# Kernel tuning notes

Hardware: AMD Instinct MI355X
Metric: run time of the kernel (lower is better)

## Reference

```python
import jax, jax.numpy as jnp
import numpy as np

N, E, IN, HID, HEADS, OUT = 50000, 800000, 128, 32, 4, 2
NEG = 0.2   # LeakyReLU negative slope (PyG default)
EPS = 1e-5  # BatchNorm eps


def setup_inputs() -> dict:
    key = jax.random.key(0)
    ks = jax.random.split(key, 32)
    g = lambda i, shape, s=0.05: (jax.random.normal(ks[i], shape, jnp.float32) * s)
    d = {
        'x': jax.random.normal(ks[0], (N, IN), jnp.float32),
        'edge_index': jax.random.randint(ks[1], (2, E), 0, N, jnp.int32),
        'edge_attr': jax.random.normal(ks[2], (E, 1), jnp.float32),
        # conv1: GATv2, in=IN, out=HID, heads=HEADS, edge_dim=1
        'c1_Wl': g(3, (IN, HEADS * HID)), 'c1_bl': g(4, (HEADS * HID,)),
        'c1_Wr': g(5, (IN, HEADS * HID)), 'c1_br': g(6, (HEADS * HID,)),
        'c1_We': g(7, (1, HEADS * HID)),
        'c1_att': g(8, (HEADS, HID)),
        'c1_bias': g(9, (HEADS * HID,)),
        'bn1_gamma': jnp.ones((HEADS * HID,), jnp.float32),
        'bn1_beta': jnp.zeros((HEADS * HID,), jnp.float32),
        'bn1_mean': g(10, (HEADS * HID,)),
        'bn1_var': jax.random.uniform(ks[11], (HEADS * HID,), jnp.float32, 0.5, 1.5),
        # conv2: GATv2, in=HEADS*HID, out=HID, heads=1, edge_dim=1
        'c2_Wl': g(12, (HEADS * HID, HID)), 'c2_bl': g(13, (HID,)),
        'c2_Wr': g(14, (HEADS * HID, HID)), 'c2_br': g(15, (HID,)),
        'c2_We': g(16, (1, HID)),
        'c2_att': g(17, (1, HID)),
        'c2_bias': g(18, (HID,)),
        'bn2_gamma': jnp.ones((HID,), jnp.float32),
        'bn2_beta': jnp.zeros((HID,), jnp.float32),
        'bn2_mean': g(19, (HID,)),
        'bn2_var': jax.random.uniform(ks[20], (HID,), jnp.float32, 0.5, 1.5),
        # classifier
        'clf_W': g(21, (HID, OUT)), 'clf_b': g(22, (OUT,)),
    }
    return d


def _gatv2(x, src, dst, eattr, Wl, bl, Wr, br, We, att, bias, heads, out_ch, concat):
    n = x.shape[0]
    xl = (x @ Wl + bl).reshape(n, heads, out_ch)   # source transform
    xr = (x @ Wr + br).reshape(n, heads, out_ch)   # target transform
    el = (eattr @ We).reshape(-1, heads, out_ch)   # edge transform (no bias in PyG)
    s = xl[src] + xr[dst] + el                     # [E, H, C]
    s = jnp.where(s > 0, s, NEG * s)               # LeakyReLU
    logits = jnp.einsum('ehc,hc->eh', s, att)      # [E, H]
    # segment softmax over destination nodes (every node has a self-loop)
    m = jax.ops.segment_max(logits, dst, num_segments=n)
    a = jnp.exp(logits - m[dst])
    denom = jax.ops.segment_sum(a, dst, num_segments=n)
    alpha = a / denom[dst]                         # [E, H]
    out = jax.ops.segment_sum(alpha[:, :, None] * xl[src], dst, num_segments=n)
    out = out.reshape(n, heads * out_ch) if concat else out.mean(axis=1)
    return out + bias


def _bn_eval(x, gamma, beta, mean, var):
    return (x - mean) * (gamma / jnp.sqrt(var + EPS)) + beta


def reference(x, edge_index, edge_attr,
              c1_Wl, c1_bl, c1_Wr, c1_br, c1_We, c1_att, c1_bias,
              bn1_gamma, bn1_beta, bn1_mean, bn1_var,
              c2_Wl, c2_bl, c2_Wr, c2_br, c2_We, c2_att, c2_bias,
              bn2_gamma, bn2_beta, bn2_mean, bn2_var,
              clf_W, clf_b):
    n = x.shape[0]
    # add self-loops once (PyG GATv2 default add_self_loops=True, fill_value='mean')
    loop = jnp.arange(n, dtype=edge_index.dtype)
    src = jnp.concatenate([edge_index[0], loop])
    dst = jnp.concatenate([edge_index[1], loop])
    loop_attr = jnp.broadcast_to(edge_attr.mean(axis=0, keepdims=True), (n, edge_attr.shape[1]))
    eattr = jnp.concatenate([edge_attr, loop_attr], axis=0)

    h = _gatv2(x, src, dst, eattr, c1_Wl, c1_bl, c1_Wr, c1_br, c1_We, c1_att, c1_bias,
               HEADS, HID, True)
    h = jax.nn.relu(_bn_eval(h, bn1_gamma, bn1_beta, bn1_mean, bn1_var))
    # dropout inactive in eval mode
    h = _gatv2(h, src, dst, eattr, c2_Wl, c2_bl, c2_Wr, c2_br, c2_We, c2_att, c2_bias,
               1, HID, True)
    h = jax.nn.relu(_bn_eval(h, bn2_gamma, bn2_beta, bn2_mean, bn2_var))
    return h @ clf_W + clf_b
```

## Files before the change

kernel.cpp:

```cpp
#include <hip/hip_runtime.h>

#define NNODES 50000
#define NEDGES 800000
#define ETOT   850000
#define IN_CH  128
#define HID    32
#define C1     128
#define NEG    0.2f
#define BNEPS  1e-5f
#define XFB2   1563
#define EHB    3125
#define WTS    160
#define XSS    136
#define NC     16
#define SCB    196

typedef __attribute__((ext_vector_type(8))) short short8;
typedef __attribute__((ext_vector_type(4))) float f32x4;

__device__ __forceinline__ unsigned short bf16r(float f) {
    unsigned u = __float_as_uint(f);
    return (unsigned short)((u + 0x7fffu + ((u >> 16) & 1u)) >> 16);
}
__device__ __forceinline__ unsigned bf16pair(float f0, float f1) {
    return (unsigned)bf16r(f0) | ((unsigned)bf16r(f1) << 16);
}
__device__ __forceinline__ float blo(unsigned u) { return __uint_as_float(u << 16); }
__device__ __forceinline__ float bhi(unsigned u) { return __uint_as_float(u & 0xffff0000u); }

__device__ __forceinline__ int block_iscan(int v, int* ls) {
    int lane = threadIdx.x & 63, w = threadIdx.x >> 6;
    #pragma unroll
    for (int o = 1; o < 64; o <<= 1) {
        int t = __shfl_up(v, o);
        if (lane >= o) v += t;
    }
    if (lane == 63) ls[w] = v;
    __syncthreads();
    int add = 0;
    #pragma unroll
    for (int i = 0; i < 4; i++) add += (i < w) ? ls[i] : 0;
    return v + add;
}

__global__ __launch_bounds__(256) void k_prep(const float* __restrict__ Wl1,
                                              const float* __restrict__ Wr1,
                                              const float* __restrict__ Wl2,
                                              const float* __restrict__ Wr2,
                                              unsigned short* __restrict__ WT,
                                              unsigned short* __restrict__ WT2,
                                              int* __restrict__ hist,
                                              float* __restrict__ meanbuf) {
    int idx = blockIdx.x * 256 + threadIdx.x;
    if (idx == 0) meanbuf[0] = 0.f;
    for (int i = idx; i < NC * NNODES; i += 160 * 256) hist[i] = 0;
    if (idx < 32768) {
        int mat = idx >> 14, rem = idx & 16383;
        int k = rem >> 7, n = rem & 127;
        float v = mat ? Wr1[k * 128 + n] : Wl1[k * 128 + n];
        WT[(size_t)(mat * 128 + n) * WTS + k] = bf16r(v);
    } else {
        int i2 = idx - 32768;
        int mat = i2 >> 12, rem = i2 & 4095;
        int k = rem >> 5, n = rem & 31;
        float v = mat ? Wr2[k * 32 + n] : Wl2[k * 32 + n];
        WT2[(size_t)(mat * 32 + n) * WTS + k] = bf16r(v);
    }
}

__global__ __launch_bounds__(256) void k_xf_eh(
    const float* __restrict__ x,
    const float* __restrict__ bl, const float* __restrict__ br,
    const unsigned short* __restrict__ WT,
    unsigned* __restrict__ xlb, float* __restrict__ xr,
    const int* __restrict__ ei, const float* __restrict__ ea,
    int* __restrict__ hist, int* __restrict__ eoff,
    float* __restrict__ meanbuf) {
    __shared__ short xs_s[64 * XSS];
    int bi = blockIdx.x;
    if (bi % 3 != 0) {
        float* ls = (float*)xs_s;
        int hb = bi - bi / 3 - 1;
        if (hb >= EHB) return;
        int e = hb * 256 + threadIdx.x;
        int c = hb & (NC - 1);
        float v = 0.f;
        if (e < NEDGES) {
            eoff[e] = atomicAdd(&hist[c * NNODES + ei[NEDGES + e]], 1);
            v = ea[e];
        }
        #pragma unroll
        for (int o = 32; o > 0; o >>= 1) v += __shfl_down(v, o, 64);
        if ((threadIdx.x & 63) == 0) ls[threadIdx.x >> 6] = v;
        __syncthreads();
        if (threadIdx.x == 0) atomicAdd(meanbuf, ls[0] + ls[1] + ls[2] + ls[3]);
        return;
    }
    int n0g = (bi / 3) * 32;
    {
        int nd = threadIdx.x >> 3, kc = (threadIdx.x & 7) * 16;
        bool valid = (n0g + nd) < NNODES;
        float xv[16];
        #pragma unroll
        for (int i = 0; i < 4; i++) {
            float4 t = valid ? ((const float4*)(x + (size_t)(n0g + nd) * IN_CH + kc))[i]
                             : make_float4(0.f, 0.f, 0.f, 0.f);
            xv[4 * i] = t.x; xv[4 * i + 1] = t.y; xv[4 * i + 2] = t.z; xv[4 * i + 3] = t.w;
        }
        unsigned hi[8], lo[8];
        #pragma unroll
        for (int i = 0; i < 8; i++) {
            unsigned short h0 = bf16r(xv[2 * i]), h1 = bf16r(xv[2 * i + 1]);
            float l0 = xv[2 * i]     - __uint_as_float(((unsigned)h0) << 16);
            float l1 = xv[2 * i + 1] - __uint_as_float(((unsigned)h1) << 16);
            hi[i] = (unsigned)h0 | ((unsigned)h1 << 16);
            lo[i] = bf16pair(l0, l1);
        }
        uint4* ph = (uint4*)&xs_s[nd * XSS + kc];
        ph[0] = make_uint4(hi[0], hi[1], hi[2], hi[3]);
        ph[1] = make_uint4(hi[4], hi[5], hi[6], hi[7]);
        uint4* pl = (uint4*)&xs_s[(nd + 32) * XSS + kc];
        pl[0] = make_uint4(lo[0], lo[1], lo[2], lo[3]);
        pl[1] = make_uint4(lo[4], lo[5], lo[6], lo[7]);
    }
    __syncthreads();
    int lane = threadIdx.x & 63;
    int lm = lane & 15, q = lane >> 4;
    int w = threadIdx.x >> 6;
    int n0 = w * 64;
    f32x4 acc[2][4];
    #pragma unroll
    for (int mt = 0; mt < 2; mt++)
        #pragma unroll
        for (int nt = 0; nt < 4; nt++) acc[mt][nt] = (f32x4)0.f;

    #pragma unroll
    for (int ks = 0; ks < 4; ks++) {
        int k0 = ks * 32 + q * 8;
        short8 ah0 = *(const short8*)&xs_s[(lm)      * XSS + k0];
        short8 ah1 = *(const short8*)&xs_s[(16 + lm) * XSS + k0];
        short8 al0 = *(const short8*)&xs_s[(32 + lm) * XSS + k0];
        short8 al1 = *(const short8*)&xs_s[(48 + lm) * XSS + k0];
        #pragma unroll
        for (int nt = 0; nt < 4; nt++) {
            short8 bfr = *(const short8*)(WT + (size_t)(n0 + nt * 16 + lm) * WTS + k0);
            acc[0][nt] = __builtin_amdgcn_mfma_f32_16x16x32_bf16(al0, bfr, acc[0][nt], 0, 0, 0);
            acc[0][nt] = __builtin_amdgcn_mfma_f32_16x16x32_bf16(ah0, bfr, acc[0][nt], 0, 0, 0);
            acc[1][nt] = __builtin_amdgcn_mfma_f32_16x16x32_bf16(al1, bfr, acc[1][nt], 0, 0, 0);
            acc[1][nt] = __builtin_amdgcn_mfma_f32_16x16x32_bf16(ah1, bfr, acc[1][nt], 0, 0, 0);
        }
    }
    if (w < 2) {
        #pragma unroll
        for (int nt = 0; nt < 4; nt++) {
            int ch = n0 + nt * 16 + lm;
            float bv = bl[ch];
            #pragma unroll
            for (int mt = 0; mt < 2; mt++)
                #pragma unroll
                for (int r = 0; r < 4; r++) {
                    int node = n0g + mt * 16 + q * 4 + r;
                    float val = acc[mt][nt][r] + bv;
                    float pv = __shfl_xor(val, 1);
                    if ((lm & 1) == 0 && node < NNODES)
                        xlb[(size_t)node * 64 + (ch >> 1)] = bf16pair(val, pv);
                }
        }
    } else {
        #pragma unroll
        for (int nt = 0; nt < 4; nt++) {
            int ch = n0 - 128 + nt * 16 + lm;
            float bv = br[ch];
            #pragma unroll
            for (int mt = 0; mt < 2; mt++)
                #pragma unroll
                for (int r = 0; r < 4; r++) {
                    int node = n0g + mt * 16 + q * 4 + r;
                    if (node < NNODES)
                        xr[(size_t)node * C1 + ch] = acc[mt][nt][r] + bv;
                }
        }
    }
}

__global__ __launch_bounds__(256) void k_red(int* __restrict__ hist,
                                             int* __restrict__ deg,
                                             int* __restrict__ bsum) {
    __shared__ int ls[4];
    int d = blockIdx.x * 256 + threadIdx.x;
    int s = 0;
    if (d < NNODES) {
        #pragma unroll
        for (int c = 0; c < NC; c++) {
            int v = hist[c * NNODES + d];
            hist[c * NNODES + d] = s;
            s += v;
        }
        deg[d] = s;
    }
    int v = (d < NNODES) ? s + 1 : 0;
    #pragma unroll
    for (int o = 32; o > 0; o >>= 1) v += __shfl_down(v, o, 64);
    if ((threadIdx.x & 63) == 0) ls[threadIdx.x >> 6] = v;
    __syncthreads();
    if (threadIdx.x == 0) bsum[blockIdx.x] = ls[0] + ls[1] + ls[2] + ls[3];
}

__global__ __launch_bounds__(256) void k_rowp(const int* __restrict__ deg,
                                              const int* __restrict__ bsum,
                                              int* __restrict__ rowptr) {
    __shared__ int ls[4];
    int t = threadIdx.x;
    int bv = (t < SCB) ? bsum[t] : 0;
    int bincl = block_iscan(bv, ls);
    __shared__ int boffs[256];
    boffs[t] = bincl - bv;
    __syncthreads();
    int base = boffs[blockIdx.x];
    __syncthreads();
    int d = blockIdx.x * 256 + t;
    int v = (d < NNODES) ? deg[d] + 1 : 0;
    int incl = block_iscan(v, ls);
    if (d < NNODES) rowptr[d] = base + incl - v;
    if (d == NNODES - 1) rowptr[NNODES] = base + incl;
}

__global__ __launch_bounds__(256) void k_fill(const int* __restrict__ ei,
                                              const float* __restrict__ ea,
                                              const int* __restrict__ rowptr,
                                              const float* __restrict__ meanbuf,
                                              const int* __restrict__ hist,
                                              const int* __restrict__ eoff,
                                              unsigned* __restrict__ cpack) {
    int e = blockIdx.x * 256 + threadIdx.x;
    if (e < NEDGES) {
        int d = ei[NEDGES + e];
        int c = (e >> 8) & (NC - 1);
        int pos = rowptr[d] + 1 + hist[c * NNODES + d] + eoff[e];
        cpack[pos] = ((unsigned)bf16r(ea[e]) << 16) | (unsigned)ei[e];
    } else if (e < NEDGES + NNODES) {
        int i = e - NEDGES;
        cpack[rowptr[i]] = ((unsigned)bf16r(meanbuf[0] * (1.0f / NEDGES)) << 16) | (unsigned)i;
    } else if (e < NEDGES + NNODES + 64) {
        cpack[ETOT + e - NEDGES - NNODES] = 0u;
    }
}

__global__ __launch_bounds__(256) void k_edge1(
    const unsigned* __restrict__ xlb, const float* __restrict__ xr,
    const int* __restrict__ rowptr, const unsigned* __restrict__ cpack,
    const float* __restrict__ We, const float* __restrict__ att,
    float* __restrict__ out1) {
    int node = blockIdx.x * 4 + (threadIdx.x >> 6);
    if (node >= NNODES) return;
    int lane = threadIdx.x & 63;
    int q = lane & 15, s = lane >> 4;
    int r0 = rowptr[node], r1 = rowptr[node + 1];
    float4 xr0 = ((const float4*)xr)[(size_t)node * 32 + 2 * q];
    float4 xr1 = ((const float4*)xr)[(size_t)node * 32 + 2 * q + 1];
    float4 we0 = ((const float4*)We)[2 * q],  we1 = ((const float4*)We)[2 * q + 1];
    float4 at0 = ((const float4*)att)[2 * q], at1 = ((const float4*)att)[2 * q + 1];
    const uint4* xlv = (const uint4*)xlb;

    float den = 0.f;
    float a0 = 0.f, a1 = 0.f, a2 = 0.f, a3 = 0.f;
    float a4 = 0.f, a5 = 0.f, a6 = 0.f, a7 = 0.f;
    int nit = (r1 - r0 + 3) >> 2;
    int k = r0 + s;
    unsigned sc0 = cpack[k];
    uint4 xv0 = xlv[(size_t)(sc0 & 0xffffu) * 16 + q];
    unsigned sc1 = cpack[k + 4];
    uint4 xv1 = xlv[(size_t)(sc1 & 0xffffu) * 16 + q];
    for (int it = 0; it < nit; it++) {
        unsigned scn = cpack[k + 8];
        uint4 xvn = xlv[(size_t)(scn & 0xffffu) * 16 + q];
        bool ok = k < r1;
        float av = __uint_as_float(sc0 & 0xffff0000u);
        float x0 = blo(xv0.x), x1 = bhi(xv0.x), x2 = blo(xv0.y), x3 = bhi(xv0.y);
        float x4 = blo(xv0.z), x5 = bhi(xv0.z), x6 = blo(xv0.w), x7 = bhi(xv0.w);
        float v0 = x0 + xr0.x + av * we0.x;  v0 = v0 > 0.f ? v0 : NEG * v0;
        float v1 = x1 + xr0.y + av * we0.y;  v1 = v1 > 0.f ? v1 : NEG * v1;
        float v2 = x2 + xr0.z + av * we0.z;  v2 = v2 > 0.f ? v2 : NEG * v2;
        float v3 = x3 + xr0.w + av * we0.w;  v3 = v3 > 0.f ? v3 : NEG * v3;
        float v4 = x4 + xr1.x + av * we1.x;  v4 = v4 > 0.f ? v4 : NEG * v4;
        float v5 = x5 + xr1.y + av * we1.y;  v5 = v5 > 0.f ? v5 : NEG * v5;
        float v6 = x6 + xr1.z + av * we1.z;  v6 = v6 > 0.f ? v6 : NEG * v6;
        float v7 = x7 + xr1.w + av * we1.w;  v7 = v7 > 0.f ? v7 : NEG * v7;
        float t = v0 * at0.x + v1 * at0.y + v2 * at0.z + v3 * at0.w
                + v4 * at1.x + v5 * at1.y + v6 * at1.z + v7 * at1.w;
        t += __shfl_xor(t, 1);
        t += __shfl_xor(t, 2);
        float e = ok ? __expf(t) : 0.f;
        den += e;
        a0 = fmaf(e, x0, a0); a1 = fmaf(e, x1, a1);
        a2 = fmaf(e, x2, a2); a3 = fmaf(e, x3, a3);
        a4 = fmaf(e, x4, a4); a5 = fmaf(e, x5, a5);
        a6 = fmaf(e, x6, a6); a7 = fmaf(e, x7, a7);
        k += 4;
        sc0 = sc1; xv0 = xv1;
        sc1 = scn; xv1 = xvn;
    }
    #pragma unroll
    for (int o = 16; o <= 32; o <<= 1) {
        den += __shfl_xor(den, o);
        a0 += __shfl_xor(a0, o); a1 += __shfl_xor(a1, o);
        a2 += __shfl_xor(a2, o); a3 += __shfl_xor(a3, o);
        a4 += __shfl_xor(a4, o); a5 += __shfl_xor(a5, o);
        a6 += __shfl_xor(a6, o); a7 += __shfl_xor(a7, o);
    }
    if (s == 0) {
        float rd = 1.f / den;
        ((float4*)out1)[(size_t)node * 32 + 2 * q] =
            make_float4(a0 * rd, a1 * rd, a2 * rd, a3 * rd);
        ((float4*)out1)[(size_t)node * 32 + 2 * q + 1] =
            make_float4(a4 * rd, a5 * rd, a6 * rd, a7 * rd);
    }
}

__global__ __launch_bounds__(256) void k_epi(
    const float* __restrict__ out1, const float* __restrict__ bias1,
    const float* __restrict__ g1, const float* __restrict__ b1,
    const float* __restrict__ m1, const float* __restrict__ v1,
    const unsigned short* __restrict__ WT2,
    const float* __restrict__ bl2, const float* __restrict__ br2,
    unsigned* __restrict__ xlb2, float* __restrict__ xr2) {
    __shared__ short hs_s[64 * XSS];
    __shared__ float A[128], B[128];
    int n0g = blockIdx.x * 32;
    if (threadIdx.x < 128) {
        int c = threadIdx.x;
        float sc = g1[c] * rsqrtf(v1[c] + BNEPS);
        A[c] = sc;
        B[c] = (bias1[c] - m1[c]) * sc + b1[c];
    }
    __syncthreads();
    {
        int nd = threadIdx.x >> 3, kc = (threadIdx.x & 7) * 16;
        bool valid = (n0g + nd) < NNODES;
        float xv[16];
        #pragma unroll
        for (int i = 0; i < 4; i++) {
            float4 t = valid ? ((const float4*)(out1 + (size_t)(n0g + nd) * C1 + kc))[i]
                             : make_float4(0.f, 0.f, 0.f, 0.f);
            xv[4 * i] = t.x; xv[4 * i + 1] = t.y; xv[4 * i + 2] = t.z; xv[4 * i + 3] = t.w;
        }
        #pragma unroll
        for (int j = 0; j < 16; j++)
            xv[j] = fmaxf(xv[j] * A[kc + j] + B[kc + j], 0.f);
        unsigned hi[8], lo[8];
        #pragma unroll
        for (int i = 0; i < 8; i++) {
            unsigned short h0 = bf16r(xv[2 * i]), h1 = bf16r(xv[2 * i + 1]);
            float l0 = xv[2 * i]     - __uint_as_float(((unsigned)h0) << 16);
            float l1 = xv[2 * i + 1] - __uint_as_float(((unsigned)h1) << 16);
            hi[i] = (unsigned)h0 | ((unsigned)h1 << 16);
            lo[i] = bf16pair(l0, l1);
        }
        uint4* ph = (uint4*)&hs_s[nd * XSS + kc];
        ph[0] = make_uint4(hi[0], hi[1], hi[2], hi[3]);
        ph[1] = make_uint4(hi[4], hi[5], hi[6], hi[7]);
        uint4* pl = (uint4*)&hs_s[(nd + 32) * XSS + kc];
        pl[0] = make_uint4(lo[0], lo[1], lo[2], lo[3]);
        pl[1] = make_uint4(lo[4], lo[5], lo[6], lo[7]);
    }
    __syncthreads();
    int lane = threadIdx.x & 63;
    int lm = lane & 15, q = lane >> 4;
    int w = threadIdx.x >> 6;
    f32x4 acc[2];
    acc[0] = (f32x4)0.f; acc[1] = (f32x4)0.f;
    #pragma unroll
    for (int ks = 0; ks < 4; ks++) {
        int k0 = ks * 32 + q * 8;
        short8 ah0 = *(const short8*)&hs_s[(lm)      * XSS + k0];
        short8 ah1 = *(const short8*)&hs_s[(16 + lm) * XSS + k0];
        short8 al0 = *(const short8*)&hs_s[(32 + lm) * XSS + k0];
        short8 al1 = *(const short8*)&hs_s[(48 + lm) * XSS + k0];
        short8 bfr = *(const short8*)(WT2 + (size_t)(w * 16 + lm) * WTS + k0);
        acc[0] = __builtin_amdgcn_mfma_f32_16x16x32_bf16(al0, bfr, acc[0], 0, 0, 0);
        acc[0] = __builtin_amdgcn_mfma_f32_16x16x32_bf16(ah0, bfr, acc[0], 0, 0, 0);
        acc[1] = __builtin_amdgcn_mfma_f32_16x16x32_bf16(al1, bfr, acc[1], 0, 0, 0);
        acc[1] = __builtin_amdgcn_mfma_f32_16x16x32_bf16(ah1, bfr, acc[1], 0, 0, 0);
    }
    if (w < 2) {
        int ch = w * 16 + lm;
        float bv = bl2[ch];
        #pragma unroll
        for (int mt = 0; mt < 2; mt++)
            #pragma unroll
            for (int r = 0; r < 4; r++) {
                int node = n0g + mt * 16 + q * 4 + r;
                float val = acc[mt][r] + bv;
                float pv = __shfl_xor(val, 1);
                if ((lm & 1) == 0 && node < NNODES)
                    xlb2[(size_t)node * 16 + (ch >> 1)] = bf16pair(val, pv);
            }
    } else {
        int ch = (w - 2) * 16 + lm;
        float bv = br2[ch];
        #pragma unroll
        for (int mt = 0; mt < 2; mt++)
            #pragma unroll
            for (int r = 0; r < 4; r++) {
                int node = n0g + mt * 16 + q * 4 + r;
                if (node < NNODES)
                    xr2[(size_t)node * HID + ch] = acc[mt][r] + bv;
            }
    }
}

__global__ __launch_bounds__(256) void k_edge2(
    const unsigned* __restrict__ xlb2, const float* __restrict__ xr2,
    const int* __restrict__ rowptr, const unsigned* __restrict__ cpack,
    const float* __restrict__ We2, const float* __restrict__ att2,
    const float* __restrict__ bias2,
    const float* __restrict__ g2, const float* __restrict__ b2,
    const float* __restrict__ m2, const float* __restrict__ v2,
    const float* __restrict__ W, const float* __restrict__ b,
    float* __restrict__ y) {
    int node = blockIdx.x * 4 + (threadIdx.x >> 6);
    if (node >= NNODES) return;
    int lane = threadIdx.x & 63;
    int q = lane & 3, s = lane >> 2;
    int r0 = rowptr[node], r1 = rowptr[node + 1];
    float4 xr0 = ((const float4*)xr2)[(size_t)node * 8 + 2 * q];
    float4 xr1 = ((const float4*)xr2)[(size_t)node * 8 + 2 * q + 1];
    float4 we0 = ((const float4*)We2)[2 * q],  we1 = ((const float4*)We2)[2 * q + 1];
    float4 at0 = ((const float4*)att2)[2 * q], at1 = ((const float4*)att2)[2 * q + 1];
    const uint4* xlv = (const uint4*)xlb2;

    float den = 0.f;
    float a0 = 0.f, a1 = 0.f, a2 = 0.f, a3 = 0.f;
    float a4 = 0.f, a5 = 0.f, a6 = 0.f, a7 = 0.f;
    int nit = (r1 - r0 + 15) >> 4;
    int k = r0 + s;
    unsigned sc = cpack[k];
    uint4 xv = xlv[(size_t)(sc & 0xffffu) * 4 + q];
    for (int it = 0; it < nit; it++) {
        unsigned scn = cpack[k + 16];
        uint4 xvn = xlv[(size_t)(scn & 0xffffu) * 4 + q];
        bool ok = k < r1;
        float av = __uint_as_float(sc & 0xffff0000u);
        float x0 = blo(xv.x), x1 = bhi(xv.x), x2 = blo(xv.y), x3 = bhi(xv.y);
        float x4 = blo(xv.z), x5 = bhi(xv.z), x6 = blo(xv.w), x7 = bhi(xv.w);
        float v0 = x0 + xr0.x + av * we0.x;  v0 = v0 > 0.f ? v0 : NEG * v0;
        float v1 = x1 + xr0.y + av * we0.y;  v1 = v1 > 0.f ? v1 : NEG * v1;
        float v2 = x2 + xr0.z + av * we0.z;  v2 = v2 > 0.f ? v2 : NEG * v2;
        float v3 = x3 + xr0.w + av * we0.w;  v3 = v3 > 0.f ? v3 : NEG * v3;
        float v4 = x4 + xr1.x + av * we1.x;  v4 = v4 > 0.f ? v4 : NEG * v4;
        float v5 = x5 + xr1.y + av * we1.y;  v5 = v5 > 0.f ? v5 : NEG * v5;
        float v6 = x6 + xr1.z + av * we1.z;  v6 = v6 > 0.f ? v6 : NEG * v6;
        float v7 = x7 + xr1.w + av * we1.w;  v7 = v7 > 0.f ? v7 : NEG * v7;
        float t = v0 * at0.x + v1 * at0.y + v2 * at0.z + v3 * at0.w
                + v4 * at1.x + v5 * at1.y + v6 * at1.z + v7 * at1.w;
        t += __shfl_xor(t, 1);
        t += __shfl_xor(t, 2);
        float e = ok ? __expf(t) : 0.f;
        den += e;
        a0 = fmaf(e, x0, a0); a1 = fmaf(e, x1, a1);
        a2 = fmaf(e, x2, a2); a3 = fmaf(e, x3, a3);
        a4 = fmaf(e, x4, a4); a5 = fmaf(e, x5, a5);
        a6 = fmaf(e, x6, a6); a7 = fmaf(e, x7, a7);
        k += 16; sc = scn; xv = xvn;
    }
    #pragma unroll
    for (int o = 4; o <= 32; o <<= 1) {
        den += __shfl_xor(den, o);
        a0 += __shfl_xor(a0, o); a1 += __shfl_xor(a1, o);
        a2 += __shfl_xor(a2, o); a3 += __shfl_xor(a3, o);
        a4 += __shfl_xor(a4, o); a5 += __shfl_xor(a5, o);
        a6 += __shfl_xor(a6, o); a7 += __shfl_xor(a7, o);
    }
    float rd = 1.f / den;
    float4 gv0 = ((const float4*)g2)[2 * q],    gv1 = ((const float4*)g2)[2 * q + 1];
    float4 bv0 = ((const float4*)b2)[2 * q],    bv1 = ((const float4*)b2)[2 * q + 1];
    float4 mv0 = ((const float4*)m2)[2 * q],    mv1 = ((const float4*)m2)[2 * q + 1];
    float4 vv0 = ((const float4*)v2)[2 * q],    vv1 = ((const float4*)v2)[2 * q + 1];
    float4 bi0 = ((const float4*)bias2)[2 * q], bi1 = ((const float4*)bias2)[2 * q + 1];
    float h0 = (a0 * rd + bi0.x - mv0.x) * (gv0.x * rsqrtf(vv0.x + BNEPS)) + bv0.x;
    float h1 = (a1 * rd + bi0.y - mv0.y) * (gv0.y * rsqrtf(vv0.y + BNEPS)) + bv0.y;
    float h2 = (a2 * rd + bi0.z - mv0.z) * (gv0.z * rsqrtf(vv0.z + BNEPS)) + bv0.z;
    float h3 = (a3 * rd + bi0.w - mv0.w) * (gv0.w * rsqrtf(vv0.w + BNEPS)) + bv0.w;
    float h4 = (a4 * rd + bi1.x - mv1.x) * (gv1.x * rsqrtf(vv1.x + BNEPS)) + bv1.x;
    float h5 = (a5 * rd + bi1.y - mv1.y) * (gv1.y * rsqrtf(vv1.y + BNEPS)) + bv1.y;
    float h6 = (a6 * rd + bi1.z - mv1.z) * (gv1.z * rsqrtf(vv1.z + BNEPS)) + bv1.z;
    float h7 = (a7 * rd + bi1.w - mv1.w) * (gv1.w * rsqrtf(vv1.w + BNEPS)) + bv1.w;
    h0 = fmaxf(h0, 0.f); h1 = fmaxf(h1, 0.f); h2 = fmaxf(h2, 0.f); h3 = fmaxf(h3, 0.f);
    h4 = fmaxf(h4, 0.f); h5 = fmaxf(h5, 0.f); h6 = fmaxf(h6, 0.f); h7 = fmaxf(h7, 0.f);
    float4 w0 = ((const float4*)W)[4 * q];
    float4 w1 = ((const float4*)W)[4 * q + 1];
    float4 w2 = ((const float4*)W)[4 * q + 2];
    float4 w3 = ((const float4*)W)[4 * q + 3];
    float t0 = h0 * w0.x + h1 * w0.z + h2 * w1.x + h3 * w1.z
             + h4 * w2.x + h5 * w2.z + h6 * w3.x + h7 * w3.z;
    float t1 = h0 * w0.y + h1 * w0.w + h2 * w1.y + h3 * w1.w
             + h4 * w2.y + h5 * w2.w + h6 * w3.y + h7 * w3.w;
    t0 += __shfl_xor(t0, 1); t0 += __shfl_xor(t0, 2);
    t1 += __shfl_xor(t1, 1); t1 += __shfl_xor(t1, 2);
    if (lane == 0) {
        y[(size_t)node * 2]     = t0 + b[0];
        y[(size_t)node * 2 + 1] = t1 + b[1];
    }
}

extern "C" void kernel_launch(void* const* d_in, const int* in_sizes, int n_in,
                              void* d_out, int out_size, void* d_ws, size_t ws_size,
                              hipStream_t stream) {
    const float* x       = (const float*)d_in[0];
    const int*   ei      = (const int*)d_in[1];
    const float* ea      = (const float*)d_in[2];
    const float* c1_Wl   = (const float*)d_in[3];
    const float* c1_bl   = (const float*)d_in[4];
    const float* c1_Wr   = (const float*)d_in[5];
    const float* c1_br   = (const float*)d_in[6];
    const float* c1_We   = (const float*)d_in[7];
    const float* c1_att  = (const float*)d_in[8];
    const float* c1_bias = (const float*)d_in[9];
    const float* bn1_g   = (const float*)d_in[10];
    const float* bn1_b   = (const float*)d_in[11];
    const float* bn1_m   = (const float*)d_in[12];
    const float* bn1_v   = (const float*)d_in[13];
    const float* c2_Wl   = (const float*)d_in[14];
    const float* c2_bl   = (const float*)d_in[15];
    const float* c2_Wr   = (const float*)d_in[16];
    const float* c2_br   = (const float*)d_in[17];
    const float* c2_We   = (const float*)d_in[18];
    const float* c2_att  = (const float*)d_in[19];
    const float* c2_bias = (const float*)d_in[20];
    const float* bn2_g   = (const float*)d_in[21];
    const float* bn2_b   = (const float*)d_in[22];
    const float* bn2_m   = (const float*)d_in[23];
    const float* bn2_v   = (const float*)d_in[24];
    const float* clf_W   = (const float*)d_in[25];
    const float* clf_b   = (const float*)d_in[26];

    float* ws = (float*)d_ws;
    size_t off = 0;
    unsigned* XLb  = (unsigned*)(ws + off); off += (size_t)NNODES * 64;
    float*    XR1  = ws + off; off += (size_t)NNODES * C1;
    float*    OUT1 = ws + off; off += (size_t)NNODES * C1;
    unsigned* XLb2 = (unsigned*)(ws + off); off += (size_t)NNODES * 16;
    float*    XR2  = ws + off; off += (size_t)NNODES * HID;
    unsigned* CPACK= (unsigned*)(ws + off); off += (size_t)ETOT + 64;
    unsigned short* WT  = (unsigned short*)(ws + off); off += 256 * WTS / 2;
    unsigned short* WT2 = (unsigned short*)(ws + off); off += 64 * WTS / 2;
    int*      EOFF = (int*)(ws + off); off += NEDGES;
    int*      ROWP = (int*)(ws + off); off += NNODES + 16;
    int*      DEG  = (int*)(ws + off); off += NNODES;
    int*      BSUM = (int*)(ws + off); off += 256;
    int*      HIST = (int*)(ws + off); off += (size_t)NC * NNODES;
    float*    MEANB= ws + off; off += 64;
    if (ws_size < off * sizeof(float)) return;

    k_prep  <<<160, 256, 0, stream>>>(c1_Wl, c1_Wr, c2_Wl, c2_Wr, WT, WT2, HIST, MEANB);
    k_xf_eh <<<3 * XFB2, 256, 0, stream>>>(x, c1_bl, c1_br, WT, XLb, XR1,
                                           ei, ea, HIST, EOFF, MEANB);
    k_red   <<<SCB, 256, 0, stream>>>(HIST, DEG, BSUM);
    k_rowp  <<<SCB, 256, 0, stream>>>(DEG, BSUM, ROWP);
    k_fill  <<<(NEDGES + NNODES + 64 + 255) / 256, 256, 0, stream>>>(ei, ea, ROWP, MEANB, HIST, EOFF, CPACK);
    k_edge1 <<<(NNODES + 3) / 4, 256, 0, stream>>>(XLb, XR1, ROWP, CPACK, c1_We, c1_att, OUT1);
    k_epi   <<<XFB2, 256, 0, stream>>>(OUT1, c1_bias, bn1_g, bn1_b, bn1_m, bn1_v,
                                       WT2, c2_bl, c2_br, XLb2, XR2);
    k_edge2 <<<(NNODES + 3) / 4, 256, 0, stream>>>(XLb2, XR2, ROWP, CPACK, c2_We, c2_att,
                                                   c2_bias, bn2_g, bn2_b, bn2_m, bn2_v,
                                                   clf_W, clf_b, (float*)d_out);
}
```

Before: 303.5 us.

## Coarsen edge-histogram/fill work per thread and make edge kernels persistent grid-stride

Histogram blocks in k_xf_eh now process four edges per thread, so the fused launch has fewer blocks and the interleave is flipped (histogram block first in each triple). k_fill is split into edge and self-loop block ranges, each doing four items per thread with loads batched ahead of stores. Both edge-attention kernels become persistent with a fixed 2048-block grid, looping over nodes and prefetching the next node's row pointers and xr, and edge2 hoists its BatchNorm scale/shift constants out of the node loop. This targets block launch overhead and latency stalls, at the risk of load imbalance from skewed node degrees under a static stride.

```diff
diff --git a/kernel.cpp b/kernel.cpp
--- a/kernel.cpp
+++ b/kernel.cpp
@@ -9,11 +9,15 @@
 #define NEG    0.2f
 #define BNEPS  1e-5f
 #define XFB2   1563
-#define EHB    3125
+#define HB4    782
 #define WTS    160
 #define XSS    136
 #define NC     16
 #define SCB    196
+#define FEB    782
+#define FLB    49
+#define EB1    2048
+#define EB2    2048
 
 typedef __attribute__((ext_vector_type(8))) short short8;
 typedef __attribute__((ext_vector_type(4))) float f32x4;
@@ -78,16 +82,29 @@
     float* __restrict__ meanbuf) {
     __shared__ short xs_s[64 * XSS];
     int bi = blockIdx.x;
-    if (bi % 3 != 0) {
+    if (bi % 3 == 0) {
         float* ls = (float*)xs_s;
-        int hb = bi - bi / 3 - 1;
-        if (hb >= EHB) return;
-        int e = hb * 256 + threadIdx.x;
-        int c = hb & (NC - 1);
+        int hb = bi / 3;
+        int e0 = hb * 1024 + threadIdx.x;
         float v = 0.f;
-        if (e < NEDGES) {
-            eoff[e] = atomicAdd(&hist[c * NNODES + ei[NEDGES + e]], 1);
-            v = ea[e];
+        if (hb < HB4 - 1) {
+            #pragma unroll
+            for (int j = 0; j < 4; j++) {
+                int e = e0 + 256 * j;
+                int c = (4 * hb + j) & (NC - 1);
+                eoff[e] = atomicAdd(&hist[c * NNODES + ei[NEDGES + e]], 1);
+                v += ea[e];
+            }
+        } else {
+            #pragma unroll
+            for (int j = 0; j < 4; j++) {
+                int e = e0 + 256 * j;
+                if (e < NEDGES) {
+                    int c = (4 * hb + j) & (NC - 1);
+                    eoff[e] = atomicAdd(&hist[c * NNODES + ei[NEDGES + e]], 1);
+                    v += ea[e];
+                }
+            }
         }
         #pragma unroll
         for (int o = 32; o > 0; o >>= 1) v += __shfl_down(v, o, 64);
@@ -96,7 +113,9 @@
         if (threadIdx.x == 0) atomicAdd(meanbuf, ls[0] + ls[1] + ls[2] + ls[3]);
         return;
     }
-    int n0g = (bi / 3) * 32;
+    int g = bi - bi / 3 - 1;
+    if (g >= XFB2) return;
+    int n0g = g * 32;
     {
         int nd = threadIdx.x >> 3, kc = (threadIdx.x & 7) * 16;
         bool valid = (n0g + nd) < NNODES;
@@ -232,18 +251,54 @@
                                               const int* __restrict__ hist,
                                               const int* __restrict__ eoff,
                                               unsigned* __restrict__ cpack) {
-    int e = blockIdx.x * 256 + threadIdx.x;
-    if (e < NEDGES) {
-        int d = ei[NEDGES + e];
-        int c = (e >> 8) & (NC - 1);
-        int pos = rowptr[d] + 1 + hist[c * NNODES + d] + eoff[e];
-        cpack[pos] = ((unsigned)bf16r(ea[e]) << 16) | (unsigned)ei[e];
-    } else if (e < NEDGES + NNODES) {
-        int i = e - NEDGES;
-        cpack[rowptr[i]] = ((unsigned)bf16r(meanbuf[0] * (1.0f / NEDGES)) << 16) | (unsigned)i;
-    } else if (e < NEDGES + NNODES + 64) {
-        cpack[ETOT + e - NEDGES - NNODES] = 0u;
-    }
+    int blk = blockIdx.x, tid = threadIdx.x;
+    if (blk < FEB) {
+        int e0 = blk * 1024 + tid;
+        int d[4], sv[4], rp[4], hs[4], eo[4];
+        float av[4];
+        bool ok[4];
+        #pragma unroll
+        for (int j = 0; j < 4; j++) {
+            int e = e0 + 256 * j;
+            ok[j] = e < NEDGES;
+            int es = ok[j] ? e : 0;
+            d[j]  = ei[NEDGES + es];
+            sv[j] = ei[es];
+            av[j] = ea[es];
+            eo[j] = eoff[es];
+        }
+        #pragma unroll
+        for (int j = 0; j < 4; j++) {
+            int e = e0 + 256 * j;
+            int c = (e >> 8) & (NC - 1);
+            rp[j] = rowptr[d[j]];
+            hs[j] = hist[c * NNODES + d[j]];
+        }
+        #pragma unroll
+        for (int j = 0; j < 4; j++)
+            if (ok[j])
+                cpack[rp[j] + 1 + hs[j] + eo[j]] =
+                    ((unsigned)bf16r(av[j]) << 16) | (unsigned)sv[j];
+        return;
+    }
+    if (blk < FEB + FLB) {
+        float mv = meanbuf[0] * (1.0f / NEDGES);
+        unsigned mp = ((unsigned)bf16r(mv)) << 16;
+        int i0 = (blk - FEB) * 1024 + tid;
+        int rp[4];
+        bool ok[4];
+        #pragma unroll
+        for (int j = 0; j < 4; j++) {
+            int i = i0 + 256 * j;
+            ok[j] = i < NNODES;
+            rp[j] = rowptr[ok[j] ? i : 0];
+        }
+        #pragma unroll
+        for (int j = 0; j < 4; j++)
+            if (ok[j]) cpack[rp[j]] = mp | (unsigned)(i0 + 256 * j);
+        return;
+    }
+    if (tid < 64) cpack[ETOT + tid] = 0u;
 }
 
 __global__ __launch_bounds__(256) void k_edge1(
@@ -251,69 +306,83 @@
     const int* __restrict__ rowptr, const unsigned* __restrict__ cpack,
     const float* __restrict__ We, const float* __restrict__ att,
     float* __restrict__ out1) {
+    int lane = threadIdx.x & 63;
+    int q = lane & 15, s = lane >> 4;
     int node = blockIdx.x * 4 + (threadIdx.x >> 6);
     if (node >= NNODES) return;
-    int lane = threadIdx.x & 63;
-    int q = lane & 15, s = lane >> 4;
+    const int W = EB1 * 4;
+    float4 we0 = ((const float4*)We)[2 * q],  we1 = ((const float4*)We)[2 * q + 1];
+    float4 at0 = ((const float4*)att)[2 * q], at1 = ((const float4*)att)[2 * q + 1];
+    const uint4* xlv = (const uint4*)xlb;
     int r0 = rowptr[node], r1 = rowptr[node + 1];
     float4 xr0 = ((const float4*)xr)[(size_t)node * 32 + 2 * q];
     float4 xr1 = ((const float4*)xr)[(size_t)node * 32 + 2 * q + 1];
-    float4 we0 = ((const float4*)We)[2 * q],  we1 = ((const float4*)We)[2 * q + 1];
-    float4 at0 = ((const float4*)att)[2 * q], at1 = ((const float4*)att)[2 * q + 1];
-    const uint4* xlv = (const uint4*)xlb;
-
-    float den = 0.f;
-    float a0 = 0.f, a1 = 0.f, a2 = 0.f, a3 = 0.f;
-    float a4 = 0.f, a5 = 0.f, a6 = 0.f, a7 = 0.f;
-    int nit = (r1 - r0 + 3) >> 2;
-    int k = r0 + s;
-    unsigned sc0 = cpack[k];
-    uint4 xv0 = xlv[(size_t)(sc0 & 0xffffu) * 16 + q];
-    unsigned sc1 = cpack[k + 4];
-    uint4 xv1 = xlv[(size_t)(sc1 & 0xffffu) * 16 + q];
-    for (int it = 0; it < nit; it++) {
-        unsigned scn = cpack[k + 8];
-        uint4 xvn = xlv[(size_t)(scn & 0xffffu) * 16 + q];
-        bool ok = k < r1;
-        float av = __uint_as_float(sc0 & 0xffff0000u);
-        float x0 = blo(xv0.x), x1 = bhi(xv0.x), x2 = blo(xv0.y), x3 = bhi(xv0.y);
-        float x4 = blo(xv0.z), x5 = bhi(xv0.z), x6 = blo(xv0.w), x7 = bhi(xv0.w);
-        float v0 = x0 + xr0.x + av * we0.x;  v0 = v0 > 0.f ? v0 : NEG * v0;
-        float v1 = x1 + xr0.y + av * we0.y;  v1 = v1 > 0.f ? v1 : NEG * v1;
-        float v2 = x2 + xr0.z + av * we0.z;  v2 = v2 > 0.f ? v2 : NEG * v2;
-        float v3 = x3 + xr0.w + av * we0.w;  v3 = v3 > 0.f ? v3 : NEG * v3;
-        float v4 = x4 + xr1.x + av * we1.x;  v4 = v4 > 0.f ? v4 : NEG * v4;
-        float v5 = x5 + xr1.y + av * we1.y;  v5 = v5 > 0.f ? v5 : NEG * v5;
-        float v6 = x6 + xr1.z + av * we1.z;  v6 = v6 > 0.f ? v6 : NEG * v6;
-        float v7 = x7 + xr1.w + av * we1.w;  v7 = v7 > 0.f ? v7 : NEG * v7;
-        float t = v0 * at0.x + v1 * at0.y + v2 * at0.z + v3 * at0.w
-                + v4 * at1.x + v5 * at1.y + v6 * at1.z + v7 * at1.w;
-        t += __shfl_xor(t, 1);
-        t += __shfl_xor(t, 2);
-        float e = ok ? __expf(t) : 0.f;
-        den += e;
-        a0 = fmaf(e, x0, a0); a1 = fmaf(e, x1, a1);
-        a2 = fmaf(e, x2, a2); a3 = fmaf(e, x3, a3);
-        a4 = fmaf(e, x4, a4); a5 = fmaf(e, x5, a5);
-        a6 = fmaf(e, x6, a6); a7 = fmaf(e, x7, a7);
-        k += 4;
-        sc0 = sc1; xv0 = xv1;
-        sc1 = scn; xv1 = xvn;
-    }
-    #pragma unroll
-    for (int o = 16; o <= 32; o <<= 1) {
-        den += __shfl_xor(den, o);
-        a0 += __shfl_xor(a0, o); a1 += __shfl_xor(a1, o);
-        a2 += __shfl_xor(a2, o); a3 += __shfl_xor(a3, o);
-        a4 += __shfl_xor(a4, o); a5 += __shfl_xor(a5, o);
-        a6 += __shfl_xor(a6, o); a7 += __shfl_xor(a7, o);
-    }
-    if (s == 0) {
-        float rd = 1.f / den;
-        ((float4*)out1)[(size_t)node * 32 + 2 * q] =
-            make_float4(a0 * rd, a1 * rd, a2 * rd, a3 * rd);
-        ((float4*)out1)[(size_t)node * 32 + 2 * q + 1] =
-            make_float4(a4 * rd, a5 * rd, a6 * rd, a7 * rd);
+    for (;;) {
+        int nn = node + W;
+        bool more = nn < NNODES;
+        int nr0 = 0, nr1 = 0;
+        float4 nxr0 = make_float4(0.f, 0.f, 0.f, 0.f);
+        float4 nxr1 = make_float4(0.f, 0.f, 0.f, 0.f);
+        if (more) {
+            nr0 = rowptr[nn]; nr1 = rowptr[nn + 1];
+            nxr0 = ((const float4*)xr)[(size_t)nn * 32 + 2 * q];
+            nxr1 = ((const float4*)xr)[(size_t)nn * 32 + 2 * q + 1];
+        }
+        float den = 0.f;
+        float a0 = 0.f, a1 = 0.f, a2 = 0.f, a3 = 0.f;
+        float a4 = 0.f, a5 = 0.f, a6 = 0.f, a7 = 0.f;
+        int nit = (r1 - r0 + 3) >> 2;
+        int k = r0 + s;
+        unsigned sc0 = cpack[k];
+        uint4 xv0 = xlv[(size_t)(sc0 & 0xffffu) * 16 + q];
+        unsigned sc1 = cpack[k + 4];
+        uint4 xv1 = xlv[(size_t)(sc1 & 0xffffu) * 16 + q];
+        for (int it = 0; it < nit; it++) {
+            unsigned scn = cpack[k + 8];
+            uint4 xvn = xlv[(size_t)(scn & 0xffffu) * 16 + q];
+            bool ok = k < r1;
+            float av = __uint_as_float(sc0 & 0xffff0000u);
+            float x0 = blo(xv0.x), x1 = bhi(xv0.x), x2 = blo(xv0.y), x3 = bhi(xv0.y);
+            float x4 = blo(xv0.z), x5 = bhi(xv0.z), x6 = blo(xv0.w), x7 = bhi(xv0.w);
+            float v0 = x0 + xr0.x + av * we0.x;  v0 = v0 > 0.f ? v0 : NEG * v0;
+            float v1 = x1 + xr0.y + av * we0.y;  v1 = v1 > 0.f ? v1 : NEG * v1;
+            float v2 = x2 + xr0.z + av * we0.z;  v2 = v2 > 0.f ? v2 : NEG * v2;
+            float v3 = x3 + xr0.w + av * we0.w;  v3 = v3 > 0.f ? v3 : NEG * v3;
+            float v4 = x4 + xr1.x + av * we1.x;  v4 = v4 > 0.f ? v4 : NEG * v4;
+            float v5 = x5 + xr1.y + av * we1.y;  v5 = v5 > 0.f ? v5 : NEG * v5;
+            float v6 = x6 + xr1.z + av * we1.z;  v6 = v6 > 0.f ? v6 : NEG * v6;
+            float v7 = x7 + xr1.w + av * we1.w;  v7 = v7 > 0.f ? v7 : NEG * v7;
+            float t = v0 * at0.x + v1 * at0.y + v2 * at0.z + v3 * at0.w
+                    + v4 * at1.x + v5 * at1.y + v6 * at1.z + v7 * at1.w;
+            t += __shfl_xor(t, 1);
+            t += __shfl_xor(t, 2);
+            float e = ok ? __expf(t) : 0.f;
+            den += e;
+            a0 = fmaf(e, x0, a0); a1 = fmaf(e, x1, a1);
+            a2 = fmaf(e, x2, a2); a3 = fmaf(e, x3, a3);
+            a4 = fmaf(e, x4, a4); a5 = fmaf(e, x5, a5);
+            a6 = fmaf(e, x6, a6); a7 = fmaf(e, x7, a7);
+            k += 4;
+            sc0 = sc1; xv0 = xv1;
+            sc1 = scn; xv1 = xvn;
+        }
+        #pragma unroll
+        for (int o = 16; o <= 32; o <<= 1) {
+            den += __shfl_xor(den, o);
+            a0 += __shfl_xor(a0, o); a1 += __shfl_xor(a1, o);
+            a2 += __shfl_xor(a2, o); a3 += __shfl_xor(a3, o);
+            a4 += __shfl_xor(a4, o); a5 += __shfl_xor(a5, o);
+            a6 += __shfl_xor(a6, o); a7 += __shfl_xor(a7, o);
+        }
+        if (s == 0) {
+            float rd = 1.f / den;
+            ((float4*)out1)[(size_t)node * 32 + 2 * q] =
+                make_float4(a0 * rd, a1 * rd, a2 * rd, a3 * rd);
+            ((float4*)out1)[(size_t)node * 32 + 2 * q + 1] =
+                make_float4(a4 * rd, a5 * rd, a6 * rd, a7 * rd);
+        }
+        if (!more) return;
+        node = nn; r0 = nr0; r1 = nr1; xr0 = nxr0; xr1 = nxr1;
     }
 }
 
@@ -418,88 +487,110 @@
     const float* __restrict__ m2, const float* __restrict__ v2,
     const float* __restrict__ W, const float* __restrict__ b,
     float* __restrict__ y) {
+    int lane = threadIdx.x & 63;
+    int q = lane & 3, s = lane >> 2;
     int node = blockIdx.x * 4 + (threadIdx.x >> 6);
     if (node >= NNODES) return;
-    int lane = threadIdx.x & 63;
-    int q = lane & 3, s = lane >> 2;
-    int r0 = rowptr[node], r1 = rowptr[node + 1];
-    float4 xr0 = ((const float4*)xr2)[(size_t)node * 8 + 2 * q];
-    float4 xr1 = ((const float4*)xr2)[(size_t)node * 8 + 2 * q + 1];
+    const int WV = EB2 * 4;
     float4 we0 = ((const float4*)We2)[2 * q],  we1 = ((const float4*)We2)[2 * q + 1];
     float4 at0 = ((const float4*)att2)[2 * q], at1 = ((const float4*)att2)[2 * q + 1];
-    const uint4* xlv = (const uint4*)xlb2;
-
-    float den = 0.f;
-    float a0 = 0.f, a1 = 0.f, a2 = 0.f, a3 = 0.f;
-    float a4 = 0.f, a5 = 0.f, a6 = 0.f, a7 = 0.f;
-    int nit = (r1 - r0 + 15) >> 4;
-    int k = r0 + s;
-    unsigned sc = cpack[k];
-    uint4 xv = xlv[(size_t)(sc & 0xffffu) * 4 + q];
-    for (int it = 0; it < nit; it++) {
-        unsigned scn = cpack[k + 16];
-        uint4 xvn = xlv[(size_t)(scn & 0xffffu) * 4 + q];
-        bool ok = k < r1;
-        float av = __uint_as_float(sc & 0xffff0000u);
-        float x0 = blo(xv.x), x1 = bhi(xv.x), x2 = blo(xv.y), x3 = bhi(xv.y);
-        float x4 = blo(xv.z), x5 = bhi(xv.z), x6 = blo(xv.w), x7 = bhi(xv.w);
-        float v0 = x0 + xr0.x + av * we0.x;  v0 = v0 > 0.f ? v0 : NEG * v0;
-        float v1 = x1 + xr0.y + av * we0.y;  v1 = v1 > 0.f ? v1 : NEG * v1;
-        float v2 = x2 + xr0.z + av * we0.z;  v2 = v2 > 0.f ? v2 : NEG * v2;
-        float v3 = x3 + xr0.w + av * we0.w;  v3 = v3 > 0.f ? v3 : NEG * v3;
-        float v4 = x4 + xr1.x + av * we1.x;  v4 = v4 > 0.f ? v4 : NEG * v4;
-        float v5 = x5 + xr1.y + av * we1.y;  v5 = v5 > 0.f ? v5 : NEG * v5;
-        float v6 = x6 + xr1.z + av * we1.z;  v6 = v6 > 0.f ? v6 : NEG * v6;
-        float v7 = x7 + xr1.w + av * we1.w;  v7 = v7 > 0.f ? v7 : NEG * v7;
-        float t = v0 * at0.x + v1 * at0.y + v2 * at0.z + v3 * at0.w
-                + v4 * at1.x + v5 * at1.y + v6 * at1.z + v7 * at1.w;
-        t += __shfl_xor(t, 1);
-        t += __shfl_xor(t, 2);
-        float e = ok ? __expf(t) : 0.f;
-        den += e;
-        a0 = fmaf(e, x0, a0); a1 = fmaf(e, x1, a1);
-        a2 = fmaf(e, x2, a2); a3 = fmaf(e, x3, a3);
-        a4 = fmaf(e, x4, a4); a5 = fmaf(e, x5, a5);
-        a6 = fmaf(e, x6, a6); a7 = fmaf(e, x7, a7);
-        k += 16; sc = scn; xv = xvn;
-    }
-    #pragma unroll
-    for (int o = 4; o <= 32; o <<= 1) {
-        den += __shfl_xor(den, o);
-        a0 += __shfl_xor(a0, o); a1 += __shfl_xor(a1, o);
-        a2 += __shfl_xor(a2, o); a3 += __shfl_xor(a3, o);
-        a4 += __shfl_xor(a4, o); a5 += __shfl_xor(a5, o);
-        a6 += __shfl_xor(a6, o); a7 += __shfl_xor(a7, o);
-    }
-    float rd = 1.f / den;
     float4 gv0 = ((const float4*)g2)[2 * q],    gv1 = ((const float4*)g2)[2 * q + 1];
     float4 bv0 = ((const float4*)b2)[2 * q],    bv1 = ((const float4*)b2)[2 * q + 1];
     float4 mv0 = ((const float4*)m2)[2 * q],    mv1 = ((const float4*)m2)[2 * q + 1];
     float4 vv0 = ((const float4*)v2)[2 * q],    vv1 = ((const float4*)v2)[2 * q + 1];
     float4 bi0 = ((const float4*)bias2)[2 * q], bi1 = ((const float4*)bias2)[2 * q + 1];
-    float h0 = (a0 * rd + bi0.x - mv0.x) * (gv0.x * rsqrtf(vv0.x + BNEPS)) + bv0.x;
-    float h1 = (a1 * rd + bi0.y - mv0.y) * (gv0.y * rsqrtf(vv0.y + BNEPS)) + bv0.y;
-    float h2 = (a2 * rd + bi0.z - mv0.z) * (gv0.z * rsqrtf(vv0.z + BNEPS)) + bv0.z;
-    float h3 = (a3 * rd + bi0.w - mv0.w) * (gv0.w * rsqrtf(vv0.w + BNEPS)) + bv0.w;
-    float h4 = (a4 * rd + bi1.x - mv1.x) * (gv1.x * rsqrtf(vv1.x + BNEPS)) + bv1.x;
-    float h5 = (a5 * rd + bi1.y - mv1.y) * (gv1.y * rsqrtf(vv1.y + BNEPS)) + bv1.y;
-    float h6 = (a6 * rd + bi1.z - mv1.z) * (gv1.z * rsqrtf(vv1.z + BNEPS)) + bv1.z;
-    float h7 = (a7 * rd + bi1.w - mv1.w) * (gv1.w * rsqrtf(vv1.w + BNEPS)) + bv1.w;
-    h0 = fmaxf(h0, 0.f); h1 = fmaxf(h1, 0.f); h2 = fmaxf(h2, 0.f); h3 = fmaxf(h3, 0.f);
-    h4 = fmaxf(h4, 0.f); h5 = fmaxf(h5, 0.f); h6 = fmaxf(h6, 0.f); h7 = fmaxf(h7, 0.f);
+    float4 sA0, sA1, sB0, sB1;
+    sA0.x = gv0.x * rsqrtf(vv0.x + BNEPS); sB0.x = (bi0.x - mv0.x) * sA0.x + bv0.x;
+    sA0.y = gv0.y * rsqrtf(vv0.y + BNEPS); sB0.y = (bi0.y - mv0.y) * sA0.y + bv0.y;
+    sA0.z = gv0.z * rsqrtf(vv0.z + BNEPS); sB0.z = (bi0.z - mv0.z) * sA0.z + bv0.z;
+    sA0.w = gv0.w * rsqrtf(vv0.w + BNEPS); sB0.w = (bi0.w - mv0.w) * sA0.w + bv0.w;
+    sA1.x = gv1.x * rsqrtf(vv1.x + BNEPS); sB1.x = (bi1.x - mv1.x) * sA1.x + bv1.x;
+    sA1.y = gv1.y * rsqrtf(vv1.y + BNEPS); sB1.y = (bi1.y - mv1.y) * sA1.y + bv1.y;
+    sA1.z = gv1.z * rsqrtf(vv1.z + BNEPS); sB1.z = (bi1.z - mv1.z) * sA1.z + bv1.z;
+    sA1.w = gv1.w * rsqrtf(vv1.w + BNEPS); sB1.w = (bi1.w - mv1.w) * sA1.w + bv1.w;
     float4 w0 = ((const float4*)W)[4 * q];
     float4 w1 = ((const float4*)W)[4 * q + 1];
     float4 w2 = ((const float4*)W)[4 * q + 2];
     float4 w3 = ((const float4*)W)[4 * q + 3];
-    float t0 = h0 * w0.x + h1 * w0.z + h2 * w1.x + h3 * w1.z
-             + h4 * w2.x + h5 * w2.z + h6 * w3.x + h7 * w3.z;
-    float t1 = h0 * w0.y + h1 * w0.w + h2 * w1.y + h3 * w1.w
-             + h4 * w2.y + h5 * w2.w + h6 * w3.y + h7 * w3.w;
-    t0 += __shfl_xor(t0, 1); t0 += __shfl_xor(t0, 2);
-    t1 += __shfl_xor(t1, 1); t1 += __shfl_xor(t1, 2);
-    if (lane == 0) {
-        y[(size_t)node * 2]     = t0 + b[0];
-        y[(size_t)node * 2 + 1] = t1 + b[1];
+    float bb0 = b[0], bb1 = b[1];
+    const uint4* xlv = (const uint4*)xlb2;
+    int r0 = rowptr[node], r1 = rowptr[node + 1];
+    float4 xr0 = ((const float4*)xr2)[(size_t)node * 8 + 2 * q];
+    float4 xr1 = ((const float4*)xr2)[(size_t)node * 8 + 2 * q + 1];
+    for (;;) {
+        int nn = node + WV;
+        bool more = nn < NNODES;
+        int nr0 = 0, nr1 = 0;
+        float4 nxr0 = make_float4(0.f, 0.f, 0.f, 0.f);
+        float4 nxr1 = make_float4(0.f, 0.f, 0.f, 0.f);
+        if (more) {
+            nr0 = rowptr[nn]; nr1 = rowptr[nn + 1];
+            nxr0 = ((const float4*)xr2)[(size_t)nn * 8 + 2 * q];
+            nxr1 = ((const float4*)xr2)[(size_t)nn * 8 + 2 * q + 1];
+        }
+        float den = 0.f;
+        float a0 = 0.f, a1 = 0.f, a2 = 0.f, a3 = 0.f;
+        float a4 = 0.f, a5 = 0.f, a6 = 0.f, a7 = 0.f;
+        int nit = (r1 - r0 + 15) >> 4;
+        int k = r0 + s;
+        unsigned sc = cpack[k];
+        uint4 xv = xlv[(size_t)(sc & 0xffffu) * 4 + q];
+        for (int it = 0; it < nit; it++) {
+            unsigned scn = cpack[k + 16];
+            uint4 xvn = xlv[(size_t)(scn & 0xffffu) * 4 + q];
+            bool ok = k < r1;
+            float av = __uint_as_float(sc & 0xffff0000u);
+            float x0 = blo(xv.x), x1 = bhi(xv.x), x2 = blo(xv.y), x3 = bhi(xv.y);
+            float x4 = blo(xv.z), x5 = bhi(xv.z), x6 = blo(xv.w), x7 = bhi(xv.w);
+            float v0 = x0 + xr0.x + av * we0.x;  v0 = v0 > 0.f ? v0 : NEG * v0;
+            float v1 = x1 + xr0.y + av * we0.y;  v1 = v1 > 0.f ? v1 : NEG * v1;
+            float v2 = x2 + xr0.z + av * we0.z;  v2 = v2 > 0.f ? v2 : NEG * v2;
+            float v3 = x3 + xr0.w + av * we0.w;  v3 = v3 > 0.f ? v3 : NEG * v3;
+            float v4 = x4 + xr1.x + av * we1.x;  v4 = v4 > 0.f ? v4 : NEG * v4;
+            float v5 = x5 + xr1.y + av * we1.y;  v5 = v5 > 0.f ? v5 : NEG * v5;
+            float v6 = x6 + xr1.z + av * we1.z;  v6 = v6 > 0.f ? v6 : NEG * v6;
+            float v7 = x7 + xr1.w + av * we1.w;  v7 = v7 > 0.f ? v7 : NEG * v7;
+            float t = v0 * at0.x + v1 * at0.y + v2 * at0.z + v3 * at0.w
+                    + v4 * at1.x + v5 * at1.y + v6 * at1.z + v7 * at1.w;
+            t += __shfl_xor(t, 1);
+            t += __shfl_xor(t, 2);
+            float e = ok ? __expf(t) : 0.f;
+            den += e;
+            a0 = fmaf(e, x0, a0); a1 = fmaf(e, x1, a1);
+            a2 = fmaf(e, x2, a2); a3 = fmaf(e, x3, a3);
+            a4 = fmaf(e, x4, a4); a5 = fmaf(e, x5, a5);
+            a6 = fmaf(e, x6, a6); a7 = fmaf(e, x7, a7);
+            k += 16; sc = scn; xv = xvn;
+        }
+        #pragma unroll
+        for (int o = 4; o <= 32; o <<= 1) {
+            den += __shfl_xor(den, o);
+            a0 += __shfl_xor(a0, o); a1 += __shfl_xor(a1, o);
+            a2 += __shfl_xor(a2, o); a3 += __shfl_xor(a3, o);
+            a4 += __shfl_xor(a4, o); a5 += __shfl_xor(a5, o);
+            a6 += __shfl_xor(a6, o); a7 += __shfl_xor(a7, o);
+        }
+        float rd = 1.f / den;
+        float h0 = fmaxf(fmaf(a0 * rd, sA0.x, sB0.x), 0.f);
+        float h1 = fmaxf(fmaf(a1 * rd, sA0.y, sB0.y), 0.f);
+        float h2 = fmaxf(fmaf(a2 * rd, sA0.z, sB0.z), 0.f);
+        float h3 = fmaxf(fmaf(a3 * rd, sA0.w, sB0.w), 0.f);
+        float h4 = fmaxf(fmaf(a4 * rd, sA1.x, sB1.x), 0.f);
+        float h5 = fmaxf(fmaf(a5 * rd, sA1.y, sB1.y), 0.f);
+        float h6 = fmaxf(fmaf(a6 * rd, sA1.z, sB1.z), 0.f);
+        float h7 = fmaxf(fmaf(a7 * rd, sA1.w, sB1.w), 0.f);
+        float t0 = h0 * w0.x + h1 * w0.z + h2 * w1.x + h3 * w1.z
+                 + h4 * w2.x + h5 * w2.z + h6 * w3.x + h7 * w3.z;
+        float t1 = h0 * w0.y + h1 * w0.w + h2 * w1.y + h3 * w1.w
+                 + h4 * w2.y + h5 * w2.w + h6 * w3.y + h7 * w3.w;
+        t0 += __shfl_xor(t0, 1); t0 += __shfl_xor(t0, 2);
+        t1 += __shfl_xor(t1, 1); t1 += __shfl_xor(t1, 2);
+        if (lane == 0) {
+            y[(size_t)node * 2]     = t0 + bb0;
+            y[(size_t)node * 2 + 1] = t1 + bb1;
+        }
+        if (!more) return;
+        node = nn; r0 = nr0; r1 = nr1; xr0 = nxr0; xr1 = nxr1;
     }
 }
 
@@ -553,15 +644,15 @@
     if (ws_size < off * sizeof(float)) return;
 
     k_prep  <<<160, 256, 0, stream>>>(c1_Wl, c1_Wr, c2_Wl, c2_Wr, WT, WT2, HIST, MEANB);
-    k_xf_eh <<<3 * XFB2, 256, 0, stream>>>(x, c1_bl, c1_br, WT, XLb, XR1,
-                                           ei, ea, HIST, EOFF, MEANB);
+    k_xf_eh <<<3 * HB4, 256, 0, stream>>>(x, c1_bl, c1_br, WT, XLb, XR1,
+                                          ei, ea, HIST, EOFF, MEANB);
     k_red   <<<SCB, 256, 0, stream>>>(HIST, DEG, BSUM);
     k_rowp  <<<SCB, 256, 0, stream>>>(DEG, BSUM, ROWP);
-    k_fill  <<<(NEDGES + NNODES + 64 + 255) / 256, 256, 0, stream>>>(ei, ea, ROWP, MEANB, HIST, EOFF, CPACK);
-    k_edge1 <<<(NNODES + 3) / 4, 256, 0, stream>>>(XLb, XR1, ROWP, CPACK, c1_We, c1_att, OUT1);
+    k_fill  <<<FEB + FLB + 1, 256, 0, stream>>>(ei, ea, ROWP, MEANB, HIST, EOFF, CPACK);
+    k_edge1 <<<EB1, 256, 0, stream>>>(XLb, XR1, ROWP, CPACK, c1_We, c1_att, OUT1);
     k_epi   <<<XFB2, 256, 0, stream>>>(OUT1, c1_bias, bn1_g, bn1_b, bn1_m, bn1_v,
                                        WT2, c2_bl, c2_br, XLb2, XR2);
-    k_edge2 <<<(NNODES + 3) / 4, 256, 0, stream>>>(XLb2, XR2, ROWP, CPACK, c2_We, c2_att,
-                                                   c2_bias, bn2_g, bn2_b, bn2_m, bn2_v,
-                                                   clf_W, clf_b, (float*)d_out);
-}
+    k_edge2 <<<EB2, 256, 0, stream>>>(XLb2, XR2, ROWP, CPACK, c2_We, c2_att,
+                                      c2_bias, bn2_g, bn2_b, bn2_m, bn2_v,
+                                      clf_W, clf_b, (float*)d_out);
+}
```

Result: faster. 294.2 us (-3.1%).
